# Kernel optimization log

Measured on AMD Instinct MI355X. Metric: run time of the kernel, lower is better.

The kernel has to match this reference:

```python
import jax, jax.numpy as jnp
import numpy as np

# pywt 'db4' decomposition low-pass filter (L = 8 taps)
_DEC_LO = np.array([
    -0.010597401784997278, 0.032883011666982945, 0.030841381835986965,
    -0.18703481171888114, -0.02798376941698385, 0.6308807679295904,
    0.7148465705525415, 0.23037781330885523], dtype=np.float32)
# pywt convention: dec_hi[n] = (-1)^(n+1) * dec_lo[L-1-n]
_SIGNS = np.array([-1.0, 1.0] * 4, dtype=np.float32)
_DEC_HI = _DEC_LO[::-1].copy() * _SIGNS

DEC_LO = jnp.asarray(_DEC_LO)
DEC_HI = jnp.asarray(_DEC_HI)
LEVELS = 3


def _dwt_per(x):
    """One level of periodization-mode DWT along axis 1.

    x: (B, N, F) with N even. Returns (cA, cD), each (B, N//2, F).
    Matches pywt: c[k] = sum_j f[j] * x[(2k + 1 - j) mod N].
    """
    N = x.shape[1]
    L = DEC_LO.shape[0]
    k = jnp.arange(N // 2)
    j = jnp.arange(L)
    idx = (2 * k[:, None] + 1 - j[None, :]) % N          # (N//2, L)
    g = x[:, idx, :]                                      # (B, N//2, L, F)
    cA = jnp.einsum('bklf,l->bkf', g, DEC_LO)
    cD = jnp.einsum('bklf,l->bkf', g, DEC_HI)
    return cA, cD


def reference(x):
    """Multilevel db4 wavedec (periodization) along axis -2 of (B, N, F).

    Returns the flat coefficient tensor (B, K, F) with pywt ordering
    [cA_L, cD_L, cD_{L-1}, ..., cD_1] concatenated along axis 1.
    """
    a = x
    details = []
    for _ in range(LEVELS):
        a, d = _dwt_per(a)
        details.append(d)
    return jnp.concatenate([a] + details[::-1], axis=1)


def setup_inputs() -> dict:
    key = jax.random.key(0)
    x = jax.random.normal(key, (64, 4096, 64), dtype=jnp.float32)
    return {"x": x}


if __name__ == "__main__":
    out = reference(**setup_inputs())
    print(out.shape)
```

## Files before the change

kernel.cpp:

```cpp
#include <hip/hip_runtime.h>


#define FV 16

__global__ __launch_bounds__(256) void dwt_level_kernel(
    const float* __restrict__ in,
    float* __restrict__ outA,
    float* __restrict__ outD,
    int N, int log2HalfN,
    int aRows, int aOff,
    int dRows, int dOff)
{
    const float LO[8] = {
        -0.010597401784997278f,  0.032883011666982945f,
         0.030841381835986965f, -0.18703481171888114f,
        -0.02798376941698385f,   0.6308807679295904f,
         0.7148465705525415f,    0.23037781330885523f};
    const float HI[8] = {
        -0.23037781330885523f,   0.7148465705525415f,
        -0.6308807679295904f,   -0.02798376941698385f,
         0.18703481171888114f,   0.030841381835986965f,
        -0.032883011666982945f, -0.010597401784997278f};

    const int halfN = 1 << log2HalfN;
    const int idx = blockIdx.x * blockDim.x + threadIdx.x;
    const int f4 = idx & (FV - 1);
    const int kb = idx >> 4;
    const int k  = kb & (halfN - 1);
    const int b  = kb >> log2HalfN;

    const float4* inB = reinterpret_cast<const float4*>(in) + (size_t)b * N * FV;

    float4 a = make_float4(0.f, 0.f, 0.f, 0.f);
    float4 d = make_float4(0.f, 0.f, 0.f, 0.f);

    const int r0 = 2 * k + 1;
#pragma unroll
    for (int j = 0; j < 8; ++j) {
        int r = r0 - j;
        if (r < 0) r += N;
        const float4 v = inB[(size_t)r * FV + f4];
        a.x = fmaf(LO[j], v.x, a.x);
        a.y = fmaf(LO[j], v.y, a.y);
        a.z = fmaf(LO[j], v.z, a.z);
        a.w = fmaf(LO[j], v.w, a.w);
        d.x = fmaf(HI[j], v.x, d.x);
        d.y = fmaf(HI[j], v.y, d.y);
        d.z = fmaf(HI[j], v.z, d.z);
        d.w = fmaf(HI[j], v.w, d.w);
    }

    reinterpret_cast<float4*>(outA)[((size_t)b * aRows + aOff + k) * FV + f4] = a;
    reinterpret_cast<float4*>(outD)[((size_t)b * dRows + dOff + k) * FV + f4] = d;
}

extern "C" void kernel_launch(void* const* d_in, const int* in_sizes, int n_in,
                              void* d_out, int out_size, void* d_ws, size_t ws_size,
                              hipStream_t stream) {
    (void)in_sizes; (void)n_in; (void)out_size; (void)ws_size;

    const float* x = (const float*)d_in[0];
    float* out = (float*)d_out;
    float* ws  = (float*)d_ws;

    const int B = 64, F = 64;
    float* cA1 = ws;
    float* cA2 = ws + (size_t)B * 2048 * F;

    {
        const int total = B * 2048 * FV;
        dwt_level_kernel<<<total / 256, 256, 0, stream>>>(
            x, cA1, out, 4096, 11, 2048, 0, 4096, 2048);
    }
    {
        const int total = B * 1024 * FV;
        dwt_level_kernel<<<total / 256, 256, 0, stream>>>(
            cA1, cA2, out, 2048, 10, 1024, 0, 4096, 1024);
    }
    {
        const int total = B * 512 * FV;
        dwt_level_kernel<<<total / 256, 256, 0, stream>>>(
            cA2, out, out, 1024, 9, 4096, 0, 4096, 512);
    }
}
```

Baseline: 128.1 us.

## Fuse three DWT levels into one streaming register-window kernel

Replaces three per-level launches that go through workspace buffers with a single kernel. Each wavefront streams a tile of input rows for one feature column and keeps sliding 8-tap windows in registers for levels 1–3, so all coefficients are computed without intermediate global round trips. Halo rows are recomputed per tile, and loads are now scalar floats rather than float4, with only 1024 blocks of 256 threads. This trades intermediate memory traffic and launch overhead for redundant halo work and lower parallelism.

```diff
diff --git a/kernel.cpp b/kernel.cpp
--- a/kernel.cpp
+++ b/kernel.cpp
@@ -1,85 +1,100 @@
 #include <hip/hip_runtime.h>
 
 
-#define FV 16
+__global__ __launch_bounds__(256) void dwt3_fused(
+    const float* __restrict__ in,
+    float* __restrict__ out)
+{
+    const float LOR[8] = { 0.23037781330885523f,   0.7148465705525415f,
+                           0.6308807679295904f,   -0.02798376941698385f,
+                          -0.18703481171888114f,   0.030841381835986965f,
+                           0.032883011666982945f, -0.010597401784997278f};
+    const float HIR[8] = {-0.010597401784997278f, -0.032883011666982945f,
+                           0.030841381835986965f,  0.18703481171888114f,
+                          -0.02798376941698385f,  -0.6308807679295904f,
+                           0.7148465705525415f,   -0.23037781330885523f};
 
-__global__ __launch_bounds__(256) void dwt_level_kernel(
-    const float* __restrict__ in,
-    float* __restrict__ outA,
-    float* __restrict__ outD,
-    int N, int log2HalfN,
-    int aRows, int aOff,
-    int dRows, int dOff)
-{
-    const float LO[8] = {
-        -0.010597401784997278f,  0.032883011666982945f,
-         0.030841381835986965f, -0.18703481171888114f,
-        -0.02798376941698385f,   0.6308807679295904f,
-         0.7148465705525415f,    0.23037781330885523f};
-    const float HI[8] = {
-        -0.23037781330885523f,   0.7148465705525415f,
-        -0.6308807679295904f,   -0.02798376941698385f,
-         0.18703481171888114f,   0.030841381835986965f,
-        -0.032883011666982945f, -0.010597401784997278f};
+    const int f    = threadIdx.x & 63;
+    const int wv   = threadIdx.x >> 6;
+    const int b    = blockIdx.x >> 4;
+    const int tile = (blockIdx.x & 15) * 4 + wv;
+    const int K3   = tile * 8;
 
-    const int halfN = 1 << log2HalfN;
-    const int idx = blockIdx.x * blockDim.x + threadIdx.x;
-    const int f4 = idx & (FV - 1);
-    const int kb = idx >> 4;
-    const int k  = kb & (halfN - 1);
-    const int b  = kb >> log2HalfN;
+    const float* inB  = in  + (size_t)b * 4096 * 64 + f;
+    float*       outB = out + (size_t)b * 4096 * 64 + f;
 
-    const float4* inB = reinterpret_cast<const float4*>(in) + (size_t)b * N * FV;
+    const int i1s = 4 * K3 - 18;
 
-    float4 a = make_float4(0.f, 0.f, 0.f, 0.f);
-    float4 d = make_float4(0.f, 0.f, 0.f, 0.f);
+    float w0[8];
+    float w1[8] = {0,0,0,0,0,0,0,0};
+    float w2[8] = {0,0,0,0,0,0,0,0};
 
-    const int r0 = 2 * k + 1;
-#pragma unroll
-    for (int j = 0; j < 8; ++j) {
-        int r = r0 - j;
-        if (r < 0) r += N;
-        const float4 v = inB[(size_t)r * FV + f4];
-        a.x = fmaf(LO[j], v.x, a.x);
-        a.y = fmaf(LO[j], v.y, a.y);
-        a.z = fmaf(LO[j], v.z, a.z);
-        a.w = fmaf(LO[j], v.w, a.w);
-        d.x = fmaf(HI[j], v.x, d.x);
-        d.y = fmaf(HI[j], v.y, d.y);
-        d.z = fmaf(HI[j], v.z, d.z);
-        d.w = fmaf(HI[j], v.w, d.w);
+    #pragma unroll
+    for (int m = 0; m < 8; ++m) {
+        const int r = (2 * i1s - 6 + m) & 4095;
+        w0[m] = inB[r * 64];
     }
 
-    reinterpret_cast<float4*>(outA)[((size_t)b * aRows + aOff + k) * FV + f4] = a;
-    reinterpret_cast<float4*>(outD)[((size_t)b * dRows + dOff + k) * FV + f4] = d;
+    #pragma unroll
+    for (int s = 0; s < 50; ++s) {
+        const int i1 = i1s + s;
+        if (s > 0) {
+            #pragma unroll
+            for (int m = 0; m < 6; ++m) w0[m] = w0[m + 2];
+            const int ra = (2 * i1)     & 4095;
+            const int rb = (2 * i1 + 1) & 4095;
+            w0[6] = inB[ra * 64];
+            w0[7] = inB[rb * 64];
+        }
+
+        float a1 = 0.f;
+        #pragma unroll
+        for (int m = 0; m < 8; ++m) a1 = fmaf(w0[m], LOR[m], a1);
+        if (s >= 18) {
+            float d1 = 0.f;
+            #pragma unroll
+            for (int m = 0; m < 8; ++m) d1 = fmaf(w0[m], HIR[m], d1);
+            outB[(size_t)((2048 + i1) & 4095) * 64] = d1;
+        }
+        #pragma unroll
+        for (int m = 0; m < 7; ++m) w1[m] = w1[m + 1];
+        w1[7] = a1;
+
+        if ((s & 1) && s >= 7) {
+            const int i2 = 2 * K3 + (s - 19) / 2;
+            float a2 = 0.f;
+            #pragma unroll
+            for (int m = 0; m < 8; ++m) a2 = fmaf(w1[m], LOR[m], a2);
+            if (s >= 19) {
+                float d2 = 0.f;
+                #pragma unroll
+                for (int m = 0; m < 8; ++m) d2 = fmaf(w1[m], HIR[m], d2);
+                outB[(size_t)((1024 + i2) & 4095) * 64] = d2;
+            }
+            #pragma unroll
+            for (int m = 0; m < 7; ++m) w2[m] = w2[m + 1];
+            w2[7] = a2;
+
+            if (s >= 21 && ((s - 21) & 3) == 0) {
+                const int i3 = K3 + (s - 21) / 4;
+                float a3 = 0.f, d3 = 0.f;
+                #pragma unroll
+                for (int m = 0; m < 8; ++m) {
+                    a3 = fmaf(w2[m], LOR[m], a3);
+                    d3 = fmaf(w2[m], HIR[m], d3);
+                }
+                outB[(size_t)(i3 & 4095) * 64]           = a3;
+                outB[(size_t)((512 + i3) & 4095) * 64]   = d3;
+            }
+        }
+    }
 }
 
 extern "C" void kernel_launch(void* const* d_in, const int* in_sizes, int n_in,
                               void* d_out, int out_size, void* d_ws, size_t ws_size,
                               hipStream_t stream) {
-    (void)in_sizes; (void)n_in; (void)out_size; (void)ws_size;
-
+    (void)in_sizes; (void)n_in; (void)out_size; (void)d_ws; (void)ws_size;
     const float* x = (const float*)d_in[0];
     float* out = (float*)d_out;
-    float* ws  = (float*)d_ws;
-
-    const int B = 64, F = 64;
-    float* cA1 = ws;
-    float* cA2 = ws + (size_t)B * 2048 * F;
-
-    {
-        const int total = B * 2048 * FV;
-        dwt_level_kernel<<<total / 256, 256, 0, stream>>>(
-            x, cA1, out, 4096, 11, 2048, 0, 4096, 2048);
-    }
-    {
-        const int total = B * 1024 * FV;
-        dwt_level_kernel<<<total / 256, 256, 0, stream>>>(
-            cA1, cA2, out, 2048, 10, 1024, 0, 4096, 1024);
-    }
-    {
-        const int total = B * 512 * FV;
-        dwt_level_kernel<<<total / 256, 256, 0, stream>>>(
-            cA2, out, out, 1024, 9, 4096, 0, 4096, 512);
-    }
+    dwt3_fused<<<1024, 256, 0, stream>>>(x, out);
 }
```

Measured after the change: 117.1 us. 1.09x faster.
